# Kernel optimization log

Hardware: AMD Instinct MI355X
Metric: run time of the kernel (lower is better)

The kernel has to match this reference:

```python
import jax, jax.numpy as jnp
import numpy as np

N_MESH = 128
BOX_SIZE = 12.8
SPACING = BOX_SIZE / N_MESH  # 0.1
N_POINTS = 100000
N_CHANNELS = 16


def setup_inputs() -> dict:
    key = jax.random.key(0)
    k1, k2 = jax.random.split(key)
    mesh_values = jax.random.normal(k1, (N_CHANNELS, N_MESH, N_MESH, N_MESH), dtype=jnp.float32)
    points = jax.random.uniform(k2, (N_POINTS, 3), dtype=jnp.float32) * BOX_SIZE
    return {"mesh_values": mesh_values, "points": points}


def reference(mesh_values, points):
    # points in real space -> fractional grid coordinates
    pc = points / SPACING                       # [N, 3]
    rp = jnp.round(pc).astype(jnp.int32)        # nearest grid point [N, 3]
    dist = pc - rp.astype(pc.dtype)             # [N, 3], in [-0.5, 0.5]
    # quadratic (order-3) interpolation weights for offsets -1, 0, +1
    w_m = (2.0 * dist - 1.0) ** 2 / 8.0
    w_0 = 0.75 - dist * dist
    w_p = (2.0 * dist + 1.0) ** 2 / 8.0
    w = jnp.stack([w_m, w_0, w_p], axis=0)      # [3, N, 3] (offset, point, axis)
    # periodic-wrapped indices for offsets -1, 0, +1
    idx = (rp[None, :, :] + jnp.array([-1, 0, 1], dtype=jnp.int32)[:, None, None]) % N_MESH  # [3, N, 3]
    # all 27 offset combinations
    ox, oy, oz = jnp.meshgrid(jnp.arange(3), jnp.arange(3), jnp.arange(3), indexing="ij")
    ox, oy, oz = ox.ravel(), oy.ravel(), oz.ravel()  # [27]
    ix = idx[ox, :, 0]  # [27, N]
    iy = idx[oy, :, 1]
    iz = idx[oz, :, 2]
    lin = (ix * N_MESH + iy) * N_MESH + iz      # [27, N] linear mesh index
    gathered = mesh_values.reshape(N_CHANNELS, -1)[:, lin]   # [C, 27, N]
    weight = w[ox, :, 0] * w[oy, :, 1] * w[oz, :, 2]          # [27, N]
    out = jnp.einsum("con,on->nc", gathered, weight)          # [N, C]
    return out
```

## Files before the change

kernel.cpp:

```cpp
#include <hip/hip_runtime.h>
#include <hip/hip_fp16.h>

#define NMESH 128
#define NMESH2 (128 * 128)
#define NMESH3 (128 * 128 * 128)
#define NPOINTS 100000
#define NCH 16

__global__ __launch_bounds__(256) void transpose_to_half_kernel(
    const float* __restrict__ in,
    __half* __restrict__ outT)
{
    __shared__ float tile[64 * 17];
    const int t = threadIdx.x;
    const int s_base = blockIdx.x * 64;
    const int lane = t & 63;
    const int c0 = t >> 6;

#pragma unroll
    for (int k = 0; k < 4; ++k) {
        const int c = c0 * 4 + k;
        tile[lane * 17 + c] = in[(size_t)c * NMESH3 + s_base + lane];
    }
    __syncthreads();

    uint32_t* out32 = (uint32_t*)(outT + (size_t)s_base * NCH);
#pragma unroll
    for (int k = 0; k < 2; ++k) {
        const int idx = t + 256 * k;
        const int s = idx >> 3;
        const int cp = idx & 7;
        const float v0 = tile[s * 17 + cp * 2];
        const float v1 = tile[s * 17 + cp * 2 + 1];
        const uint32_t packed =
            (uint32_t)__half_as_ushort(__float2half(v0)) |
            ((uint32_t)__half_as_ushort(__float2half(v1)) << 16);
        out32[s * 8 + cp] = packed;
    }
}

__global__ __launch_bounds__(256) void gather_half_kernel(
    const __half* __restrict__ meshT,
    const float* __restrict__ pts,
    float* __restrict__ out)
{
    const int tid = blockIdx.x * 256 + threadIdx.x;
    const int c = tid & (NCH - 1);
    const int p = tid >> 4;
    if (p >= NPOINTS) return;

    const float SP = 0.1f;
    const float pcx = pts[p * 3 + 0] / SP;
    const float pcy = pts[p * 3 + 1] / SP;
    const float pcz = pts[p * 3 + 2] / SP;

    const int rx = (int)rintf(pcx);
    const int ry = (int)rintf(pcy);
    const int rz = (int)rintf(pcz);

    const float dx = pcx - (float)rx;
    const float dy = pcy - (float)ry;
    const float dz = pcz - (float)rz;

    float wX[3], wY[3], wZ[3];
    wX[0] = (2.0f * dx - 1.0f) * (2.0f * dx - 1.0f) * 0.125f;
    wX[1] = 0.75f - dx * dx;
    wX[2] = (2.0f * dx + 1.0f) * (2.0f * dx + 1.0f) * 0.125f;
    wY[0] = (2.0f * dy - 1.0f) * (2.0f * dy - 1.0f) * 0.125f;
    wY[1] = 0.75f - dy * dy;
    wY[2] = (2.0f * dy + 1.0f) * (2.0f * dy + 1.0f) * 0.125f;
    wZ[0] = (2.0f * dz - 1.0f) * (2.0f * dz - 1.0f) * 0.125f;
    wZ[1] = 0.75f - dz * dz;
    wZ[2] = (2.0f * dz + 1.0f) * (2.0f * dz + 1.0f) * 0.125f;

    int xo[3], yo[3], zo[3];
#pragma unroll
    for (int k = 0; k < 3; ++k) {
        xo[k] = ((rx - 1 + k) & (NMESH - 1)) * (NMESH2 * NCH);
        yo[k] = ((ry - 1 + k) & (NMESH - 1)) * (NMESH * NCH);
        zo[k] = ((rz - 1 + k) & (NMESH - 1)) * NCH + c;
    }

    float acc = 0.0f;
#pragma unroll
    for (int a = 0; a < 3; ++a) {
#pragma unroll
        for (int b = 0; b < 3; ++b) {
            const int base = xo[a] + yo[b];
            const float wxy = wX[a] * wY[b];
            acc = fmaf(__half2float(meshT[base + zo[0]]), wxy * wZ[0], acc);
            acc = fmaf(__half2float(meshT[base + zo[1]]), wxy * wZ[1], acc);
            acc = fmaf(__half2float(meshT[base + zo[2]]), wxy * wZ[2], acc);
        }
    }

    out[tid] = acc;
}

__global__ __launch_bounds__(256) void mesh_interp_fallback_kernel(
    const float* __restrict__ mesh,
    const float* __restrict__ pts,
    float* __restrict__ out)
{
    const int tid = blockIdx.x * 256 + threadIdx.x;
    const int c = tid & (NCH - 1);
    const int p = tid >> 4;
    if (p >= NPOINTS) return;

    const float SP = 0.1f;
    const float pcx = pts[p * 3 + 0] / SP;
    const float pcy = pts[p * 3 + 1] / SP;
    const float pcz = pts[p * 3 + 2] / SP;

    const int rx = (int)rintf(pcx);
    const int ry = (int)rintf(pcy);
    const int rz = (int)rintf(pcz);

    const float dx = pcx - (float)rx;
    const float dy = pcy - (float)ry;
    const float dz = pcz - (float)rz;

    float wX[3], wY[3], wZ[3];
    wX[0] = (2.0f * dx - 1.0f) * (2.0f * dx - 1.0f) * 0.125f;
    wX[1] = 0.75f - dx * dx;
    wX[2] = (2.0f * dx + 1.0f) * (2.0f * dx + 1.0f) * 0.125f;
    wY[0] = (2.0f * dy - 1.0f) * (2.0f * dy - 1.0f) * 0.125f;
    wY[1] = 0.75f - dy * dy;
    wY[2] = (2.0f * dy + 1.0f) * (2.0f * dy + 1.0f) * 0.125f;
    wZ[0] = (2.0f * dz - 1.0f) * (2.0f * dz - 1.0f) * 0.125f;
    wZ[1] = 0.75f - dz * dz;
    wZ[2] = (2.0f * dz + 1.0f) * (2.0f * dz + 1.0f) * 0.125f;

    int xb[3], yb[3], zi[3];
#pragma unroll
    for (int k = 0; k < 3; ++k) {
        xb[k] = ((rx - 1 + k) & (NMESH - 1)) * NMESH2;
        yb[k] = ((ry - 1 + k) & (NMESH - 1)) * NMESH;
        zi[k] = ((rz - 1 + k) & (NMESH - 1));
    }

    const float* __restrict__ mc = mesh + (size_t)c * NMESH3;
    float acc = 0.0f;
#pragma unroll
    for (int a = 0; a < 3; ++a) {
#pragma unroll
        for (int b = 0; b < 3; ++b) {
            const float* __restrict__ row = mc + xb[a] + yb[b];
            const float wxy = wX[a] * wY[b];
            acc = fmaf(row[zi[0]], wxy * wZ[0], acc);
            acc = fmaf(row[zi[1]], wxy * wZ[1], acc);
            acc = fmaf(row[zi[2]], wxy * wZ[2], acc);
        }
    }
    out[tid] = acc;
}

extern "C" void kernel_launch(void* const* d_in, const int* in_sizes, int n_in,
                              void* d_out, int out_size, void* d_ws, size_t ws_size,
                              hipStream_t stream) {
    const float* mesh = (const float*)d_in[0];
    const float* pts  = (const float*)d_in[1];
    float* out        = (float*)d_out;

    const size_t needed = (size_t)NMESH3 * NCH * sizeof(__half);

    if (ws_size >= needed) {
        __half* meshT = (__half*)d_ws;
        transpose_to_half_kernel<<<NMESH3 / 64, 256, 0, stream>>>(mesh, meshT);
        const int total = NPOINTS * NCH;
        gather_half_kernel<<<(total + 255) / 256, 256, 0, stream>>>(meshT, pts, out);
    } else {
        const int total = NPOINTS * NCH;
        mesh_interp_fallback_kernel<<<(total + 255) / 256, 256, 0, stream>>>(mesh, pts, out);
    }
}
```

Measured before the change: 226.1 us.

## Vectorize transpose and gather: per-thread 16-channel transpose, 4 channels per gather thread

The transpose kernel drops the shared-memory tile: each thread now reads all 16 channels for one mesh site and writes 32 bytes of packed halves with two 16-byte stores. The gather kernel assigns 4 channels per thread, loading 8 bytes of halves per tap and storing a float4, which cuts the thread count and per-point weight recomputation by 4x. This reduces instruction count and the number of memory transactions, at the cost of higher register use and more strided per-thread reads in the transpose.

```diff
diff --git a/kernel.cpp b/kernel.cpp
--- a/kernel.cpp
+++ b/kernel.cpp
@@ -7,46 +7,37 @@
 #define NPOINTS 100000
 #define NCH 16
 
-__global__ __launch_bounds__(256) void transpose_to_half_kernel(
+__global__ __launch_bounds__(256) void transpose_to_half_v2(
     const float* __restrict__ in,
     __half* __restrict__ outT)
 {
-    __shared__ float tile[64 * 17];
-    const int t = threadIdx.x;
-    const int s_base = blockIdx.x * 64;
-    const int lane = t & 63;
-    const int c0 = t >> 6;
+    const int s = blockIdx.x * 256 + threadIdx.x;
 
+    float v[NCH];
 #pragma unroll
-    for (int k = 0; k < 4; ++k) {
-        const int c = c0 * 4 + k;
-        tile[lane * 17 + c] = in[(size_t)c * NMESH3 + s_base + lane];
+    for (int c = 0; c < NCH; ++c)
+        v[c] = in[(size_t)c * NMESH3 + s];
+
+    uint32_t u[8];
+#pragma unroll
+    for (int k = 0; k < 8; ++k) {
+        u[k] = (uint32_t)__half_as_ushort(__float2half(v[2 * k])) |
+               ((uint32_t)__half_as_ushort(__float2half(v[2 * k + 1])) << 16);
     }
-    __syncthreads();
 
-    uint32_t* out32 = (uint32_t*)(outT + (size_t)s_base * NCH);
-#pragma unroll
-    for (int k = 0; k < 2; ++k) {
-        const int idx = t + 256 * k;
-        const int s = idx >> 3;
-        const int cp = idx & 7;
-        const float v0 = tile[s * 17 + cp * 2];
-        const float v1 = tile[s * 17 + cp * 2 + 1];
-        const uint32_t packed =
-            (uint32_t)__half_as_ushort(__float2half(v0)) |
-            ((uint32_t)__half_as_ushort(__float2half(v1)) << 16);
-        out32[s * 8 + cp] = packed;
-    }
+    uint4* dst = (uint4*)(outT + (size_t)s * NCH);
+    dst[0] = make_uint4(u[0], u[1], u[2], u[3]);
+    dst[1] = make_uint4(u[4], u[5], u[6], u[7]);
 }
 
-__global__ __launch_bounds__(256) void gather_half_kernel(
+__global__ __launch_bounds__(256) void gather_half_v2(
     const __half* __restrict__ meshT,
     const float* __restrict__ pts,
     float* __restrict__ out)
 {
     const int tid = blockIdx.x * 256 + threadIdx.x;
-    const int c = tid & (NCH - 1);
-    const int p = tid >> 4;
+    const int p = tid >> 2;
+    const int c0 = (tid & 3) * 4;
     if (p >= NPOINTS) return;
 
     const float SP = 0.1f;
@@ -78,23 +69,34 @@
     for (int k = 0; k < 3; ++k) {
         xo[k] = ((rx - 1 + k) & (NMESH - 1)) * (NMESH2 * NCH);
         yo[k] = ((ry - 1 + k) & (NMESH - 1)) * (NMESH * NCH);
-        zo[k] = ((rz - 1 + k) & (NMESH - 1)) * NCH + c;
+        zo[k] = ((rz - 1 + k) & (NMESH - 1)) * NCH + c0;
     }
 
-    float acc = 0.0f;
+    float acc0 = 0.0f, acc1 = 0.0f, acc2 = 0.0f, acc3 = 0.0f;
 #pragma unroll
     for (int a = 0; a < 3; ++a) {
 #pragma unroll
         for (int b = 0; b < 3; ++b) {
             const int base = xo[a] + yo[b];
             const float wxy = wX[a] * wY[b];
-            acc = fmaf(__half2float(meshT[base + zo[0]]), wxy * wZ[0], acc);
-            acc = fmaf(__half2float(meshT[base + zo[1]]), wxy * wZ[1], acc);
-            acc = fmaf(__half2float(meshT[base + zo[2]]), wxy * wZ[2], acc);
+#pragma unroll
+            for (int k = 0; k < 3; ++k) {
+                const float2 raw = *(const float2*)(meshT + base + zo[k]);
+                const __half2 h01 = *(const __half2*)&raw.x;
+                const __half2 h23 = *(const __half2*)&raw.y;
+                const float2 f01 = __half22float2(h01);
+                const float2 f23 = __half22float2(h23);
+                const float w = wxy * wZ[k];
+                acc0 = fmaf(f01.x, w, acc0);
+                acc1 = fmaf(f01.y, w, acc1);
+                acc2 = fmaf(f23.x, w, acc2);
+                acc3 = fmaf(f23.y, w, acc3);
+            }
         }
     }
 
-    out[tid] = acc;
+    float4 res = make_float4(acc0, acc1, acc2, acc3);
+    *(float4*)(out + (size_t)p * NCH + c0) = res;
 }
 
 __global__ __launch_bounds__(256) void mesh_interp_fallback_kernel(
@@ -166,9 +168,9 @@
 
     if (ws_size >= needed) {
         __half* meshT = (__half*)d_ws;
-        transpose_to_half_kernel<<<NMESH3 / 64, 256, 0, stream>>>(mesh, meshT);
-        const int total = NPOINTS * NCH;
-        gather_half_kernel<<<(total + 255) / 256, 256, 0, stream>>>(meshT, pts, out);
+        transpose_to_half_v2<<<NMESH3 / 256, 256, 0, stream>>>(mesh, meshT);
+        const int total = NPOINTS * 4;
+        gather_half_v2<<<(total + 255) / 256, 256, 0, stream>>>(meshT, pts, out);
     } else {
         const int total = NPOINTS * NCH;
         mesh_interp_fallback_kernel<<<(total + 255) / 256, 256, 0, stream>>>(mesh, pts, out);
```

Result: no change. 226.7 us (+0.3%).
